# Kernel tuning notes

Hardware: AMD Instinct MI355X
Metric: run time of the kernel (lower is better)

Reference implementation:

```python
import jax, jax.numpy as jnp
import numpy as np

N = 6144
INPUT_SIZE = 1024
HIDDEN = 256
NEG_INF = -9e15  # matches torch masked_fill value -9000000000000000.0


def setup_inputs() -> dict:
    key = jax.random.key(0)
    k1, k2, k3, k4 = jax.random.split(key, 4)
    nodes_embed = jax.random.normal(k1, (N, INPUT_SIZE), dtype=jnp.float32)
    node_adj = jax.random.randint(k2, (N, N), 0, 2, dtype=jnp.int32)
    # learned params (xavier-uniform-ish scaling)
    limW = np.sqrt(6.0 / (INPUT_SIZE + HIDDEN))
    W = jax.random.uniform(k3, (INPUT_SIZE, HIDDEN), minval=-limW, maxval=limW, dtype=jnp.float32)
    lima = 1.414 * np.sqrt(6.0 / (2 * HIDDEN + 1))
    a_edge = jax.random.uniform(k4, (2 * HIDDEN,), minval=-lima, maxval=lima, dtype=jnp.float32)
    return {"nodes_embed": nodes_embed, "W": W, "a_edge": a_edge, "node_adj": node_adj}


def reference(nodes_embed, W, a_edge, node_adj):
    # h = nodes_embed @ W : [N, hidden]
    h = nodes_embed @ W
    # W_edge([h_i ; h_j]) decomposes exactly: (h_i @ a1) + (h_j @ a2)
    a1, a2 = a_edge[:HIDDEN], a_edge[HIDDEN:]
    score = (h @ a1)[:, None] + (h @ a2)[None, :]  # [N, N]
    adj_f = node_adj.astype(h.dtype)
    weight = jax.nn.leaky_relu(adj_f * score, negative_slope=0.2)
    weight = jnp.where(node_adj == 0, jnp.asarray(NEG_INF, h.dtype), weight)
    attention = jax.nn.softmax(weight, axis=-1)
    # dropout in eval mode (identity)
    return attention @ h  # [N, hidden]
```

## Files before the change

kernel.cpp:

```cpp
#include <hip/hip_runtime.h>
#include <hip/hip_bf16.h>

#define NN 6144
#define INPUT 1024
#define HID 256

using frag  = __attribute__((ext_vector_type(8))) short;
using f32x4 = __attribute__((ext_vector_type(4))) float;

static __device__ __forceinline__ unsigned short bf16u(float x) {
    unsigned u = __float_as_uint(x);
    u += 0x7fff + ((u >> 16) & 1);
    return (unsigned short)(u >> 16);
}

__global__ __launch_bounds__(256) void k_prep(const float* __restrict__ X,
                                              const float* __restrict__ W,
                                              unsigned short* __restrict__ Xb,
                                              unsigned short* __restrict__ Wt) {
    int b = blockIdx.x;
    if (b < 3072) {
        int t = b * 256 + threadIdx.x;
        const float4* p = reinterpret_cast<const float4*>(X) + (size_t)t * 2;
        float4 x0 = p[0], x1 = p[1];
        frag v;
        v[0] = (short)bf16u(x0.x); v[1] = (short)bf16u(x0.y);
        v[2] = (short)bf16u(x0.z); v[3] = (short)bf16u(x0.w);
        v[4] = (short)bf16u(x1.x); v[5] = (short)bf16u(x1.y);
        v[6] = (short)bf16u(x1.z); v[7] = (short)bf16u(x1.w);
        *reinterpret_cast<frag*>(Xb + (size_t)t * 8) = v;
    } else {
        int t = (b - 3072) * 256 + threadIdx.x;
        int n = t >> 10, k = t & 1023;
        Wt[t] = bf16u(W[k * HID + n]);
    }
}

__global__ __launch_bounds__(256) void k_gemm1(const unsigned short* __restrict__ Xb,
                                               const unsigned short* __restrict__ Wt,
                                               const float* __restrict__ a_edge,
                                               unsigned short* __restrict__ hT,
                                               float* __restrict__ s1,
                                               float* __restrict__ s2) {
    __shared__ unsigned short A[2][32][72];
    int t = threadIdx.x;
    int m = t >> 3, cg = t & 7;
    int i0 = blockIdx.x * 32, n0 = blockIdx.y * 64;
    int w = t >> 6, l = t & 63, lm = l & 15, q = l >> 4;
    int nw = n0 + w * 16;

    const unsigned short* xrow = Xb + (size_t)(i0 + m) * INPUT + cg * 8;
    const unsigned short* brow = Wt + (size_t)(nw + lm) * INPUT + q * 8;

    f32x4 acc0 = {}, acc1 = {};
    frag av = *reinterpret_cast<const frag*>(xrow);

    for (int c = 0; c < 16; c++) {
        int buf = c & 1;
        *reinterpret_cast<frag*>(&A[buf][m][cg * 8]) = av;
        if (c < 15) av = *reinterpret_cast<const frag*>(xrow + (c + 1) * 64);
        __syncthreads();

#pragma unroll
        for (int kk = 0; kk < 2; kk++) {
            frag a0 = *reinterpret_cast<const frag*>(&A[buf][lm][kk * 32 + q * 8]);
            frag a1 = *reinterpret_cast<const frag*>(&A[buf][16 + lm][kk * 32 + q * 8]);
            frag b  = *reinterpret_cast<const frag*>(brow + c * 64 + kk * 32);
            acc0 = __builtin_amdgcn_mfma_f32_16x16x32_bf16(a0, b, acc0, 0, 0, 0);
            acc1 = __builtin_amdgcn_mfma_f32_16x16x32_bf16(a1, b, acc1, 0, 0, 0);
        }
    }

    ushort4 o;
    o.x = bf16u(acc0[0]); o.y = bf16u(acc0[1]); o.z = bf16u(acc0[2]); o.w = bf16u(acc0[3]);
    *reinterpret_cast<ushort4*>(hT + (size_t)(nw + lm) * NN + i0 + q * 4) = o;
    o.x = bf16u(acc1[0]); o.y = bf16u(acc1[1]); o.z = bf16u(acc1[2]); o.w = bf16u(acc1[3]);
    *reinterpret_cast<ushort4*>(hT + (size_t)(nw + lm) * NN + i0 + 16 + q * 4) = o;

    float a1v = a_edge[nw + lm], a2v = a_edge[HID + nw + lm];
#pragma unroll
    for (int h = 0; h < 2; h++) {
        const f32x4& ac = h ? acc1 : acc0;
#pragma unroll
        for (int r = 0; r < 4; r++) {
            float v1 = ac[r] * a1v, v2 = ac[r] * a2v;
            v1 += __shfl_xor(v1, 1); v2 += __shfl_xor(v2, 1);
            v1 += __shfl_xor(v1, 2); v2 += __shfl_xor(v2, 2);
            v1 += __shfl_xor(v1, 4); v2 += __shfl_xor(v2, 4);
            v1 += __shfl_xor(v1, 8); v2 += __shfl_xor(v2, 8);
            if (lm == 0) {
                atomicAdd(&s1[i0 + h * 16 + q * 4 + r], v1);
                atomicAdd(&s2[i0 + h * 16 + q * 4 + r], v2);
            }
        }
    }
}

__global__ __launch_bounds__(512) void k_attn(const int* __restrict__ adj,
                                              const float* __restrict__ s1,
                                              const float* __restrict__ s2,
                                              const unsigned short* __restrict__ hT,
                                              float* __restrict__ U4,
                                              float* __restrict__ denom4) {
    __shared__ unsigned short P[2][32][136];
    int t = threadIdx.x;
    int m = t >> 4, cg = t & 15;
    int i0 = blockIdx.x * 32;
    int q4 = blockIdx.y;
    int j0 = q4 * 1536;
    int w = t >> 6, l = t & 63, lm = l & 15, q = l >> 4;

    float s1v = s1[i0 + m];
    const int*   arow = adj + (size_t)(i0 + m) * NN + j0 + cg * 8;
    const float* s2p  = s2 + j0 + cg * 8;

    const unsigned short* brow[2];
#pragma unroll
    for (int nt = 0; nt < 2; nt++)
        brow[nt] = hT + (size_t)(w * 32 + nt * 16 + lm) * NN + j0 + q * 8;

    f32x4 acc[2][2] = {};
    float dsum = 0.f;

    int4 ca0 = *reinterpret_cast<const int4*>(arow);
    int4 ca1 = *reinterpret_cast<const int4*>(arow + 4);

    for (int c = 0; c < 12; c++) {
        int buf = c & 1;
        int jc = c * 128;

        int4 na0, na1;
        if (c < 11) {
            na0 = *reinterpret_cast<const int4*>(arow + jc + 128);
            na1 = *reinterpret_cast<const int4*>(arow + jc + 132);
        }

        float4 sv0 = *reinterpret_cast<const float4*>(s2p + jc);
        float4 sv1 = *reinterpret_cast<const float4*>(s2p + jc + 4);
        float sc, wv, p0, p1, p2, p3, p4, p5, p6, p7;
        sc = s1v + sv0.x; wv = fmaxf(sc, 0.2f * sc); p0 = ca0.x ? __expf(wv) : 0.f;
        sc = s1v + sv0.y; wv = fmaxf(sc, 0.2f * sc); p1 = ca0.y ? __expf(wv) : 0.f;
        sc = s1v + sv0.z; wv = fmaxf(sc, 0.2f * sc); p2 = ca0.z ? __expf(wv) : 0.f;
        sc = s1v + sv0.w; wv = fmaxf(sc, 0.2f * sc); p3 = ca0.w ? __expf(wv) : 0.f;
        sc = s1v + sv1.x; wv = fmaxf(sc, 0.2f * sc); p4 = ca1.x ? __expf(wv) : 0.f;
        sc = s1v + sv1.y; wv = fmaxf(sc, 0.2f * sc); p5 = ca1.y ? __expf(wv) : 0.f;
        sc = s1v + sv1.z; wv = fmaxf(sc, 0.2f * sc); p6 = ca1.z ? __expf(wv) : 0.f;
        sc = s1v + sv1.w; wv = fmaxf(sc, 0.2f * sc); p7 = ca1.w ? __expf(wv) : 0.f;
        dsum += ((p0 + p1) + (p2 + p3)) + ((p4 + p5) + (p6 + p7));
        frag pk;
        pk[0] = (short)bf16u(p0); pk[1] = (short)bf16u(p1);
        pk[2] = (short)bf16u(p2); pk[3] = (short)bf16u(p3);
        pk[4] = (short)bf16u(p4); pk[5] = (short)bf16u(p5);
        pk[6] = (short)bf16u(p6); pk[7] = (short)bf16u(p7);
        *reinterpret_cast<frag*>(&P[buf][m][cg * 8]) = pk;

        __syncthreads();

        __builtin_amdgcn_s_setprio(1);
#pragma unroll
        for (int kk = 0; kk < 4; kk++) {
            frag a0 = *reinterpret_cast<const frag*>(&P[buf][lm][kk * 32 + q * 8]);
            frag a1 = *reinterpret_cast<const frag*>(&P[buf][16 + lm][kk * 32 + q * 8]);
#pragma unroll
            for (int nt = 0; nt < 2; nt++) {
                frag b = *reinterpret_cast<const frag*>(brow[nt] + jc + kk * 32);
                acc[0][nt] = __builtin_amdgcn_mfma_f32_16x16x32_bf16(a0, b, acc[0][nt], 0, 0, 0);
                acc[1][nt] = __builtin_amdgcn_mfma_f32_16x16x32_bf16(a1, b, acc[1][nt], 0, 0, 0);
            }
        }
        __builtin_amdgcn_s_setprio(0);

        ca0 = na0; ca1 = na1;
    }

    float v = dsum;
    v += __shfl_xor(v, 1); v += __shfl_xor(v, 2);
    v += __shfl_xor(v, 4); v += __shfl_xor(v, 8);
    if (cg == 0) denom4[(size_t)q4 * NN + i0 + m] = v;

    float* Ub = U4 + (size_t)q4 * NN * HID;
#pragma unroll
    for (int h = 0; h < 2; h++)
#pragma unroll
        for (int nt = 0; nt < 2; nt++)
#pragma unroll
            for (int r = 0; r < 4; r++)
                Ub[(size_t)(i0 + h * 16 + q * 4 + r) * HID + w * 32 + nt * 16 + lm] = acc[h][nt][r];
}

__global__ __launch_bounds__(256) void k_norm(const float* __restrict__ U4,
                                              const float* __restrict__ denom4,
                                              float* __restrict__ out) {
    int i = blockIdx.x, t = threadIdx.x;
    size_t S = (size_t)NN * HID;
    size_t base = (size_t)i * HID + t;
    float u = U4[base] + U4[base + S] + U4[base + 2 * S] + U4[base + 3 * S];
    float d = denom4[i] + denom4[i + NN] + denom4[i + 2 * NN] + denom4[i + 3 * NN];
    out[base] = (d != 0.f) ? u / d : 0.f;
}

extern "C" void kernel_launch(void* const* d_in, const int* in_sizes, int n_in,
                              void* d_out, int out_size, void* d_ws, size_t ws_size,
                              hipStream_t stream) {
    const float* X      = (const float*)d_in[0];
    const float* W      = (const float*)d_in[1];
    const float* a_edge = (const float*)d_in[2];
    const int*   adj    = (const int*)d_in[3];
    float* out = (float*)d_out;

    float* U4     = (float*)d_ws;
    float* denom4 = U4 + (size_t)4 * NN * HID;
    float* s1     = denom4 + (size_t)4 * NN;
    float* s2     = s1 + NN;
    unsigned short* hT = (unsigned short*)(s2 + NN);
    unsigned short* Wt = hT + (size_t)HID * NN;
    unsigned short* Xb = (unsigned short*)U4;

    hipMemsetAsync(s1, 0, 2 * NN * sizeof(float), stream);
    k_prep<<<3072 + INPUT * HID / 256, 256, 0, stream>>>(X, W, Xb, Wt);
    k_gemm1<<<dim3(NN / 32, HID / 64), 256, 0, stream>>>(Xb, Wt, a_edge, hT, s1, s2);
    k_attn<<<dim3(NN / 32, 4), 512, 0, stream>>>(adj, s1, s2, hT, U4, denom4);
    k_norm<<<NN, 256, 0, stream>>>(U4, denom4, out);
}
```

Baseline: 310.7 us.

## Compute attention probabilities directly in MFMA register layout, dropping LDS staging

The attention kernel now has each lane compute its softmax numerators directly in the MFMA A-fragment layout. This removes the shared-memory P buffer and the per-chunk __syncthreads. Blocks shrink to 256 threads, each wave covers 64 output columns, and adjacency, s2 and hT fragments are double-buffered in registers. The first GEMM likewise reads A fragments straight from global memory with register double-buffering instead of going through LDS, and bf16 packing uses the v_cvt_pk_bf16_f32 instruction. The cost is higher register pressure and redundant global loads across waves: each of the four waves in a block reloads the same adjacency and s2 data and recomputes the exponentials.

After: 389.4 us. 25.3% more time.

```diff
diff --git a/kernel.cpp b/kernel.cpp
--- a/kernel.cpp
+++ b/kernel.cpp
@@ -7,11 +7,19 @@
 
 using frag  = __attribute__((ext_vector_type(8))) short;
 using f32x4 = __attribute__((ext_vector_type(4))) float;
+
+union FU { frag f; unsigned u[4]; };
 
 static __device__ __forceinline__ unsigned short bf16u(float x) {
     unsigned u = __float_as_uint(x);
     u += 0x7fff + ((u >> 16) & 1);
     return (unsigned short)(u >> 16);
+}
+
+static __device__ __forceinline__ unsigned cvtpk(float lo, float hi) {
+    unsigned r;
+    asm("v_cvt_pk_bf16_f32 %0, %1, %2" : "=v"(r) : "v"(lo), "v"(hi));
+    return r;
 }
 
 __global__ __launch_bounds__(256) void k_prep(const float* __restrict__ X,
@@ -36,48 +44,46 @@
     }
 }
 
-__global__ __launch_bounds__(256) void k_gemm1(const unsigned short* __restrict__ Xb,
-                                               const unsigned short* __restrict__ Wt,
-                                               const float* __restrict__ a_edge,
-                                               unsigned short* __restrict__ hT,
-                                               float* __restrict__ s1,
-                                               float* __restrict__ s2) {
-    __shared__ unsigned short A[2][32][72];
+__global__ __launch_bounds__(256, 4) void k_gemm1(const unsigned short* __restrict__ Xb,
+                                                  const unsigned short* __restrict__ Wt,
+                                                  const float* __restrict__ a_edge,
+                                                  unsigned short* __restrict__ hT,
+                                                  float* __restrict__ s1,
+                                                  float* __restrict__ s2) {
     int t = threadIdx.x;
-    int m = t >> 3, cg = t & 7;
-    int i0 = blockIdx.x * 32, n0 = blockIdx.y * 64;
     int w = t >> 6, l = t & 63, lm = l & 15, q = l >> 4;
-    int nw = n0 + w * 16;
-
-    const unsigned short* xrow = Xb + (size_t)(i0 + m) * INPUT + cg * 8;
-    const unsigned short* brow = Wt + (size_t)(nw + lm) * INPUT + q * 8;
+    int i0 = blockIdx.x * 32;
+    int n0 = blockIdx.y * 64 + w * 16;
+
+    const unsigned short* arow0 = Xb + (size_t)(i0 + lm) * INPUT + q * 8;
+    const unsigned short* arow1 = arow0 + 16 * INPUT;
+    const unsigned short* brow  = Wt + (size_t)(n0 + lm) * INPUT + q * 8;
 
     f32x4 acc0 = {}, acc1 = {};
-    frag av = *reinterpret_cast<const frag*>(xrow);
-
-    for (int c = 0; c < 16; c++) {
-        int buf = c & 1;
-        *reinterpret_cast<frag*>(&A[buf][m][cg * 8]) = av;
-        if (c < 15) av = *reinterpret_cast<const frag*>(xrow + (c + 1) * 64);
-        __syncthreads();
-
-#pragma unroll
-        for (int kk = 0; kk < 2; kk++) {
-            frag a0 = *reinterpret_cast<const frag*>(&A[buf][lm][kk * 32 + q * 8]);
-            frag a1 = *reinterpret_cast<const frag*>(&A[buf][16 + lm][kk * 32 + q * 8]);
-            frag b  = *reinterpret_cast<const frag*>(brow + c * 64 + kk * 32);
-            acc0 = __builtin_amdgcn_mfma_f32_16x16x32_bf16(a0, b, acc0, 0, 0, 0);
-            acc1 = __builtin_amdgcn_mfma_f32_16x16x32_bf16(a1, b, acc1, 0, 0, 0);
+    frag A0[2], A1[2], B[2];
+    A0[0] = *reinterpret_cast<const frag*>(arow0);
+    A1[0] = *reinterpret_cast<const frag*>(arow1);
+    B[0]  = *reinterpret_cast<const frag*>(brow);
+
+#pragma unroll
+    for (int ks = 0; ks < 32; ks++) {
+        int cur = ks & 1, nxt = cur ^ 1;
+        if (ks < 31) {
+            A0[nxt] = *reinterpret_cast<const frag*>(arow0 + (ks + 1) * 32);
+            A1[nxt] = *reinterpret_cast<const frag*>(arow1 + (ks + 1) * 32);
+            B[nxt]  = *reinterpret_cast<const frag*>(brow + (ks + 1) * 32);
         }
+        acc0 = __builtin_amdgcn_mfma_f32_16x16x32_bf16(A0[cur], B[cur], acc0, 0, 0, 0);
+        acc1 = __builtin_amdgcn_mfma_f32_16x16x32_bf16(A1[cur], B[cur], acc1, 0, 0, 0);
     }
 
     ushort4 o;
     o.x = bf16u(acc0[0]); o.y = bf16u(acc0[1]); o.z = bf16u(acc0[2]); o.w = bf16u(acc0[3]);
-    *reinterpret_cast<ushort4*>(hT + (size_t)(nw + lm) * NN + i0 + q * 4) = o;
+    *reinterpret_cast<ushort4*>(hT + (size_t)(n0 + lm) * NN + i0 + q * 4) = o;
     o.x = bf16u(acc1[0]); o.y = bf16u(acc1[1]); o.z = bf16u(acc1[2]); o.w = bf16u(acc1[3]);
-    *reinterpret_cast<ushort4*>(hT + (size_t)(nw + lm) * NN + i0 + 16 + q * 4) = o;
-
-    float a1v = a_edge[nw + lm], a2v = a_edge[HID + nw + lm];
+    *reinterpret_cast<ushort4*>(hT + (size_t)(n0 + lm) * NN + i0 + 16 + q * 4) = o;
+
+    float a1v = a_edge[n0 + lm], a2v = a_edge[HID + n0 + lm];
 #pragma unroll
     for (int h = 0; h < 2; h++) {
         const f32x4& ac = h ? acc1 : acc0;
@@ -96,96 +102,116 @@
     }
 }
 
-__global__ __launch_bounds__(512) void k_attn(const int* __restrict__ adj,
-                                              const float* __restrict__ s1,
-                                              const float* __restrict__ s2,
-                                              const unsigned short* __restrict__ hT,
-                                              float* __restrict__ U4,
-                                              float* __restrict__ denom4) {
-    __shared__ unsigned short P[2][32][136];
+__global__ __launch_bounds__(256, 3) void k_attn(const int* __restrict__ adj,
+                                                 const float* __restrict__ s1,
+                                                 const float* __restrict__ s2,
+                                                 const unsigned short* __restrict__ hT,
+                                                 float* __restrict__ U4,
+                                                 float* __restrict__ denom4) {
     int t = threadIdx.x;
-    int m = t >> 4, cg = t & 15;
+    int nq = t >> 6, l = t & 63, lm = l & 15, q = l >> 4;
     int i0 = blockIdx.x * 32;
     int q4 = blockIdx.y;
     int j0 = q4 * 1536;
-    int w = t >> 6, l = t & 63, lm = l & 15, q = l >> 4;
-
-    float s1v = s1[i0 + m];
-    const int*   arow = adj + (size_t)(i0 + m) * NN + j0 + cg * 8;
-    const float* s2p  = s2 + j0 + cg * 8;
-
-    const unsigned short* brow[2];
-#pragma unroll
-    for (int nt = 0; nt < 2; nt++)
-        brow[nt] = hT + (size_t)(w * 32 + nt * 16 + lm) * NN + j0 + q * 8;
-
-    f32x4 acc[2][2] = {};
-    float dsum = 0.f;
-
-    int4 ca0 = *reinterpret_cast<const int4*>(arow);
-    int4 ca1 = *reinterpret_cast<const int4*>(arow + 4);
-
-    for (int c = 0; c < 12; c++) {
-        int buf = c & 1;
-        int jc = c * 128;
-
-        int4 na0, na1;
-        if (c < 11) {
-            na0 = *reinterpret_cast<const int4*>(arow + jc + 128);
-            na1 = *reinterpret_cast<const int4*>(arow + jc + 132);
+
+    float s1v0 = s1[i0 + lm], s1v1 = s1[i0 + 16 + lm];
+    const int*   arow0 = adj + (size_t)(i0 + lm) * NN + j0 + q * 8;
+    const int*   arow1 = arow0 + (size_t)16 * NN;
+    const float* s2p   = s2 + j0 + q * 8;
+    const unsigned short* bp0 = hT + (size_t)(nq * 64 + 0 * 16 + lm) * NN + j0 + q * 8;
+    const unsigned short* bp1 = hT + (size_t)(nq * 64 + 1 * 16 + lm) * NN + j0 + q * 8;
+    const unsigned short* bp2 = hT + (size_t)(nq * 64 + 2 * 16 + lm) * NN + j0 + q * 8;
+    const unsigned short* bp3 = hT + (size_t)(nq * 64 + 3 * 16 + lm) * NN + j0 + q * 8;
+
+    f32x4 acc[2][4] = {};
+    float dsL = 0.f, dsH = 0.f;
+
+    int4   AL0[2], AL1[2], AH0[2], AH1[2];
+    float4 S0[2], S1[2];
+    frag   Bf[2][4];
+
+#define LOADSTEP(KS, SET)                                                     \
+    {                                                                         \
+        AL0[SET] = *reinterpret_cast<const int4*>(arow0 + (KS) * 32);         \
+        AL1[SET] = *reinterpret_cast<const int4*>(arow0 + (KS) * 32 + 4);     \
+        AH0[SET] = *reinterpret_cast<const int4*>(arow1 + (KS) * 32);         \
+        AH1[SET] = *reinterpret_cast<const int4*>(arow1 + (KS) * 32 + 4);     \
+        S0[SET]  = *reinterpret_cast<const float4*>(s2p + (KS) * 32);         \
+        S1[SET]  = *reinterpret_cast<const float4*>(s2p + (KS) * 32 + 4);     \
+        Bf[SET][0] = *reinterpret_cast<const frag*>(bp0 + (KS) * 32);         \
+        Bf[SET][1] = *reinterpret_cast<const frag*>(bp1 + (KS) * 32);         \
+        Bf[SET][2] = *reinterpret_cast<const frag*>(bp2 + (KS) * 32);         \
+        Bf[SET][3] = *reinterpret_cast<const frag*>(bp3 + (KS) * 32);         \
+    }
+
+#define COMPUTE(SET)                                                                          \
+    {                                                                                         \
+        float sc, wv, pa, pb;                                                                 \
+        FU fL, fH;                                                                            \
+        sc = s1v0 + S0[SET].x; wv = fmaxf(sc, 0.2f * sc); pa = AL0[SET].x ? __expf(wv) : 0.f; \
+        sc = s1v0 + S0[SET].y; wv = fmaxf(sc, 0.2f * sc); pb = AL0[SET].y ? __expf(wv) : 0.f; \
+        dsL += pa + pb; fL.u[0] = cvtpk(pa, pb);                                              \
+        sc = s1v0 + S0[SET].z; wv = fmaxf(sc, 0.2f * sc); pa = AL0[SET].z ? __expf(wv) : 0.f; \
+        sc = s1v0 + S0[SET].w; wv = fmaxf(sc, 0.2f * sc); pb = AL0[SET].w ? __expf(wv) : 0.f; \
+        dsL += pa + pb; fL.u[1] = cvtpk(pa, pb);                                              \
+        sc = s1v0 + S1[SET].x; wv = fmaxf(sc, 0.2f * sc); pa = AL1[SET].x ? __expf(wv) : 0.f; \
+        sc = s1v0 + S1[SET].y; wv = fmaxf(sc, 0.2f * sc); pb = AL1[SET].y ? __expf(wv) : 0.f; \
+        dsL += pa + pb; fL.u[2] = cvtpk(pa, pb);                                              \
+        sc = s1v0 + S1[SET].z; wv = fmaxf(sc, 0.2f * sc); pa = AL1[SET].z ? __expf(wv) : 0.f; \
+        sc = s1v0 + S1[SET].w; wv = fmaxf(sc, 0.2f * sc); pb = AL1[SET].w ? __expf(wv) : 0.f; \
+        dsL += pa + pb; fL.u[3] = cvtpk(pa, pb);                                              \
+        sc = s1v1 + S0[SET].x; wv = fmaxf(sc, 0.2f * sc); pa = AH0[SET].x ? __expf(wv) : 0.f; \
+        sc = s1v1 + S0[SET].y; wv = fmaxf(sc, 0.2f * sc); pb = AH0[SET].y ? __expf(wv) : 0.f; \
+        dsH += pa + pb; fH.u[0] = cvtpk(pa, pb);                                              \
+        sc = s1v1 + S0[SET].z; wv = fmaxf(sc, 0.2f * sc); pa = AH0[SET].z ? __expf(wv) : 0.f; \
+        sc = s1v1 + S0[SET].w; wv = fmaxf(sc, 0.2f * sc); pb = AH0[SET].w ? __expf(wv) : 0.f; \
+        dsH += pa + pb; fH.u[1] = cvtpk(pa, pb);                                              \
+        sc = s1v1 + S1[SET].x; wv = fmaxf(sc, 0.2f * sc); pa = AH1[SET].x ? __expf(wv) : 0.f; \
+        sc = s1v1 + S1[SET].y; wv = fmaxf(sc, 0.2f * sc); pb = AH1[SET].y ? __expf(wv) : 0.f; \
+        dsH += pa + pb; fH.u[2] = cvtpk(pa, pb);                                              \
+        sc = s1v1 + S1[SET].z; wv = fmaxf(sc, 0.2f * sc); pa = AH1[SET].z ? __expf(wv) : 0.f; \
+        sc = s1v1 + S1[SET].w; wv = fmaxf(sc, 0.2f * sc); pb = AH1[SET].w ? __expf(wv) : 0.f; \
+        dsH += pa + pb; fH.u[3] = cvtpk(pa, pb);                                              \
+        acc[0][0] = __builtin_amdgcn_mfma_f32_16x16x32_bf16(fL.f, Bf[SET][0], acc[0][0], 0, 0, 0); \
+        acc[1][0] = __builtin_amdgcn_mfma_f32_16x16x32_bf16(fH.f, Bf[SET][0], acc[1][0], 0, 0, 0); \
+        acc[0][1] = __builtin_amdgcn_mfma_f32_16x16x32_bf16(fL.f, Bf[SET][1], acc[0][1], 0, 0, 0); \
+        acc[1][1] = __builtin_amdgcn_mfma_f32_16x16x32_bf16(fH.f, Bf[SET][1], acc[1][1], 0, 0, 0); \
+        acc[0][2] = __builtin_amdgcn_mfma_f32_16x16x32_bf16(fL.f, Bf[SET][2], acc[0][2], 0, 0, 0); \
+        acc[1][2] = __builtin_amdgcn_mfma_f32_16x16x32_bf16(fH.f, Bf[SET][2], acc[1][2], 0, 0, 0); \
+        acc[0][3] = __builtin_amdgcn_mfma_f32_16x16x32_bf16(fL.f, Bf[SET][3], acc[0][3], 0, 0, 0); \
+        acc[1][3] = __builtin_amdgcn_mfma_f32_16x16x32_bf16(fH.f, Bf[SET][3], acc[1][3], 0, 0, 0); \
+    }
+
+    LOADSTEP(0, 0)
+    for (int it = 0; it < 23; ++it) {
+#pragma unroll
+        for (int sub = 0; sub < 2; ++sub) {
+            int ks = it * 2 + sub;
+            LOADSTEP(ks + 1, sub ^ 1)
+            COMPUTE(sub)
         }
-
-        float4 sv0 = *reinterpret_cast<const float4*>(s2p + jc);
-        float4 sv1 = *reinterpret_cast<const float4*>(s2p + jc + 4);
-        float sc, wv, p0, p1, p2, p3, p4, p5, p6, p7;
-        sc = s1v + sv0.x; wv = fmaxf(sc, 0.2f * sc); p0 = ca0.x ? __expf(wv) : 0.f;
-        sc = s1v + sv0.y; wv = fmaxf(sc, 0.2f * sc); p1 = ca0.y ? __expf(wv) : 0.f;
-        sc = s1v + sv0.z; wv = fmaxf(sc, 0.2f * sc); p2 = ca0.z ? __expf(wv) : 0.f;
-        sc = s1v + sv0.w; wv = fmaxf(sc, 0.2f * sc); p3 = ca0.w ? __expf(wv) : 0.f;
-        sc = s1v + sv1.x; wv = fmaxf(sc, 0.2f * sc); p4 = ca1.x ? __expf(wv) : 0.f;
-        sc = s1v + sv1.y; wv = fmaxf(sc, 0.2f * sc); p5 = ca1.y ? __expf(wv) : 0.f;
-        sc = s1v + sv1.z; wv = fmaxf(sc, 0.2f * sc); p6 = ca1.z ? __expf(wv) : 0.f;
-        sc = s1v + sv1.w; wv = fmaxf(sc, 0.2f * sc); p7 = ca1.w ? __expf(wv) : 0.f;
-        dsum += ((p0 + p1) + (p2 + p3)) + ((p4 + p5) + (p6 + p7));
-        frag pk;
-        pk[0] = (short)bf16u(p0); pk[1] = (short)bf16u(p1);
-        pk[2] = (short)bf16u(p2); pk[3] = (short)bf16u(p3);
-        pk[4] = (short)bf16u(p4); pk[5] = (short)bf16u(p5);
-        pk[6] = (short)bf16u(p6); pk[7] = (short)bf16u(p7);
-        *reinterpret_cast<frag*>(&P[buf][m][cg * 8]) = pk;
-
-        __syncthreads();
-
-        __builtin_amdgcn_s_setprio(1);
-#pragma unroll
-        for (int kk = 0; kk < 4; kk++) {
-            frag a0 = *reinterpret_cast<const frag*>(&P[buf][lm][kk * 32 + q * 8]);
-            frag a1 = *reinterpret_cast<const frag*>(&P[buf][16 + lm][kk * 32 + q * 8]);
-#pragma unroll
-            for (int nt = 0; nt < 2; nt++) {
-                frag b = *reinterpret_cast<const frag*>(brow[nt] + jc + kk * 32);
-                acc[0][nt] = __builtin_amdgcn_mfma_f32_16x16x32_bf16(a0, b, acc[0][nt], 0, 0, 0);
-                acc[1][nt] = __builtin_amdgcn_mfma_f32_16x16x32_bf16(a1, b, acc[1][nt], 0, 0, 0);
-            }
-        }
-        __builtin_amdgcn_s_setprio(0);
-
-        ca0 = na0; ca1 = na1;
-    }
-
-    float v = dsum;
-    v += __shfl_xor(v, 1); v += __shfl_xor(v, 2);
-    v += __shfl_xor(v, 4); v += __shfl_xor(v, 8);
-    if (cg == 0) denom4[(size_t)q4 * NN + i0 + m] = v;
+    }
+    LOADSTEP(47, 1)
+    COMPUTE(0)
+    COMPUTE(1)
+#undef LOADSTEP
+#undef COMPUTE
+
+    dsL += __shfl_xor(dsL, 16); dsL += __shfl_xor(dsL, 32);
+    dsH += __shfl_xor(dsH, 16); dsH += __shfl_xor(dsH, 32);
+    if (nq == 0 && q == 0) {
+        denom4[(size_t)q4 * NN + i0 + lm]      = dsL;
+        denom4[(size_t)q4 * NN + i0 + 16 + lm] = dsH;
+    }
 
     float* Ub = U4 + (size_t)q4 * NN * HID;
 #pragma unroll
     for (int h = 0; h < 2; h++)
 #pragma unroll
-        for (int nt = 0; nt < 2; nt++)
+        for (int nt = 0; nt < 4; nt++)
 #pragma unroll
             for (int r = 0; r < 4; r++)
-                Ub[(size_t)(i0 + h * 16 + q * 4 + r) * HID + w * 32 + nt * 16 + lm] = acc[h][nt][r];
+                Ub[(size_t)(i0 + h * 16 + q * 4 + r) * HID + nq * 64 + nt * 16 + lm] = acc[h][nt][r];
 }
 
 __global__ __launch_bounds__(256) void k_norm(const float* __restrict__ U4,
@@ -218,7 +244,7 @@
 
     hipMemsetAsync(s1, 0, 2 * NN * sizeof(float), stream);
     k_prep<<<3072 + INPUT * HID / 256, 256, 0, stream>>>(X, W, Xb, Wt);
-    k_gemm1<<<dim3(NN / 32, HID / 64), 256, 0, stream>>>(Xb, Wt, a_edge, hT, s1, s2);
-    k_attn<<<dim3(NN / 32, 4), 512, 0, stream>>>(adj, s1, s2, hT, U4, denom4);
+    k_gemm1<<<dim3(NN / 32, 4), 256, 0, stream>>>(Xb, Wt, a_edge, hT, s1, s2);
+    k_attn<<<dim3(NN / 32, 4), 256, 0, stream>>>(adj, s1, s2, hT, U4, denom4);
     k_norm<<<NN, 256, 0, stream>>>(U4, denom4, out);
 }
```
